# Kernel optimization log

Hardware: AMD Instinct MI355X
Metric: run time of the kernel (lower is better)

Reference implementation:

```python
import jax, jax.numpy as jnp
import numpy as np

H_DIM = 2048
D_FF = 4 * H_DIM
NUM_EXPERTS = 8
NUM_SHARED = 2
BATCH, SEQ = 2, 2048


def setup_inputs() -> dict:
    key = jax.random.key(0)
    ks = jax.random.split(key, 10)
    s = 0.02
    return {
        "x": jax.random.normal(ks[0], (BATCH, SEQ, H_DIM), dtype=jnp.float32),
        "ws_w1": jax.random.normal(ks[1], (NUM_SHARED, H_DIM, D_FF), dtype=jnp.float32) * s,
        "ws_b1": jnp.zeros((NUM_SHARED, D_FF), dtype=jnp.float32),
        "ws_w2": jax.random.normal(ks[2], (NUM_SHARED, D_FF, H_DIM), dtype=jnp.float32) * s,
        "ws_b2": jnp.zeros((NUM_SHARED, H_DIM), dtype=jnp.float32),
        "we_w1": jax.random.normal(ks[3], (NUM_EXPERTS, H_DIM, D_FF), dtype=jnp.float32) * s,
        "we_b1": jnp.zeros((NUM_EXPERTS, D_FF), dtype=jnp.float32),
        "we_w2": jax.random.normal(ks[4], (NUM_EXPERTS, D_FF, H_DIM), dtype=jnp.float32) * s,
        "we_b2": jnp.zeros((NUM_EXPERTS, H_DIM), dtype=jnp.float32),
        "wg": jax.random.normal(ks[5], (H_DIM, NUM_EXPERTS), dtype=jnp.float32) * s,
        "top_k": 2,
    }


def reference(x, ws_w1, ws_b1, ws_w2, ws_b2, we_w1, we_b1, we_w2, we_b2, wg, top_k):
    B, S, D = x.shape
    xt = x.reshape(-1, D)  # [T, D], T = B*S
    T = xt.shape[0]

    # ---- shared experts: sum over NUM_SHARED dense MLPs ----
    hs = jax.nn.relu(jnp.einsum('td,ndf->ntf', xt, ws_w1) + ws_b1[:, None, :])
    shared = jnp.einsum('ntf,nfd->td', hs, ws_w2) + ws_b2.sum(axis=0)  # [T, D]

    # ---- sparse top-k routed MoE ----
    logits = xt @ wg                       # [T, E] router logits
    probs = jax.nn.softmax(logits, axis=-1)
    topv, topi = jax.lax.top_k(probs, top_k)
    gates = jnp.zeros_like(probs).at[jnp.arange(T)[:, None], topi].set(topv)  # [T, E]

    moe = jnp.zeros_like(xt)
    for e in range(we_w1.shape[0]):  # small fixed expert count
        he = jax.nn.relu(xt @ we_w1[e] + we_b1[e])
        ye = he @ we_w2[e] + we_b2[e]
        moe = moe + gates[:, e:e + 1] * ye

    out = (shared + moe).reshape(B, S, D)
    return out, logits
```

## Files before the change

kernel.cpp:

```cpp
#include <hip/hip_runtime.h>

#define TOKENS 4096
#define HD 2048
#define FF 8192
#define NE 8
#define NS 2

typedef __attribute__((ext_vector_type(8))) short bf16x8;
typedef __attribute__((ext_vector_type(4))) float f32x4;

__device__ __forceinline__ unsigned rnd_bf(unsigned u) {
  return u + 0x7fffu + ((u >> 16) & 1u);
}
__device__ __forceinline__ unsigned short f2bf(float f) {
  unsigned u = __builtin_bit_cast(unsigned, f);
  return (unsigned short)(rnd_bf(u) >> 16);
}

#define GLDS16(gp, lp)                                                         \
  __builtin_amdgcn_global_load_lds(                                            \
      (const __attribute__((address_space(1))) unsigned*)(const void*)(gp),    \
      (__attribute__((address_space(3))) unsigned*)(lp), 16, 0, 0)

__global__ void cast_x_kernel(const float* __restrict__ x, unsigned short* __restrict__ xb) {
  const size_t i = ((size_t)blockIdx.x * 256 + threadIdx.x) * 4;
  float4 v = *(const float4*)(x + i);
  ushort4 o;
  o.x = f2bf(v.x); o.y = f2bf(v.y); o.z = f2bf(v.z); o.w = f2bf(v.w);
  *(ushort4*)(xb + i) = o;
}

__global__ void router_kernel(const float* __restrict__ x, const float* __restrict__ wg,
                              float* __restrict__ logits_out, int* __restrict__ topi,
                              float* __restrict__ topv, int* __restrict__ counts) {
  const int wave = threadIdx.x >> 6, lane = threadIdx.x & 63;
  const int t = blockIdx.x * 4 + wave;
  const float* xr = x + (size_t)t * HD;
  float acc[8];
#pragma unroll
  for (int e = 0; e < 8; ++e) acc[e] = 0.f;
  for (int d = lane; d < HD; d += 64) {
    const float xv = xr[d];
    const float4 w0 = *(const float4*)(wg + (size_t)d * 8);
    const float4 w1 = *(const float4*)(wg + (size_t)d * 8 + 4);
    acc[0] += xv * w0.x; acc[1] += xv * w0.y; acc[2] += xv * w0.z; acc[3] += xv * w0.w;
    acc[4] += xv * w1.x; acc[5] += xv * w1.y; acc[6] += xv * w1.z; acc[7] += xv * w1.w;
  }
#pragma unroll
  for (int e = 0; e < 8; ++e) {
#pragma unroll
    for (int off = 32; off > 0; off >>= 1) acc[e] += __shfl_xor(acc[e], off);
  }
  if (lane == 0) {
    *(float4*)(logits_out + (size_t)t * 8)     = make_float4(acc[0], acc[1], acc[2], acc[3]);
    *(float4*)(logits_out + (size_t)t * 8 + 4) = make_float4(acc[4], acc[5], acc[6], acc[7]);
    float mx = acc[0];
#pragma unroll
    for (int e = 1; e < 8; ++e) mx = fmaxf(mx, acc[e]);
    float p[8], s = 0.f;
#pragma unroll
    for (int e = 0; e < 8; ++e) { p[e] = expf(acc[e] - mx); s += p[e]; }
    const float inv = 1.f / s;
    int i1 = 0;
#pragma unroll
    for (int e = 1; e < 8; ++e) if (acc[e] > acc[i1]) i1 = e;
    int i2 = (i1 == 0) ? 1 : 0;
#pragma unroll
    for (int e = 0; e < 8; ++e) if (e != i1 && acc[e] > acc[i2]) i2 = e;
    topi[2 * t]     = i1; topv[2 * t]     = p[i1] * inv;
    topi[2 * t + 1] = i2; topv[2 * t + 1] = p[i2] * inv;
    atomicAdd(&counts[i1], 1);
    atomicAdd(&counts[i2], 1);
  }
}

__global__ void offs_kernel(const int* __restrict__ counts, int* __restrict__ offs,
                            int* __restrict__ cursors) {
  if (threadIdx.x == 0) {
    int r = 0;
    for (int e = 0; e < NE; ++e) { offs[e] = r; cursors[e] = r; r += counts[e]; }
  }
}

__global__ void gather_kernel(const unsigned short* __restrict__ xb,
                              const int* __restrict__ topi, const float* __restrict__ topv,
                              int* __restrict__ cursors, unsigned short* __restrict__ xg,
                              int* __restrict__ row_token, float* __restrict__ row_gate) {
  const int wave = threadIdx.x >> 6, lane = threadIdx.x & 63;
  const int t = blockIdx.x * 4 + wave;
  const uint4* src = (const uint4*)(xb + (size_t)t * HD);
#pragma unroll
  for (int j = 0; j < 2; ++j) {
    const int e = topi[2 * t + j];
    int pos = 0;
    if (lane == 0) {
      pos = atomicAdd(&cursors[e], 1);
      row_token[pos] = t;
      row_gate[pos] = topv[2 * t + j];
    }
    pos = __shfl(pos, 0);
    uint4* dst = (uint4*)(xg + (size_t)pos * HD);
#pragma unroll
    for (int c = lane; c < 256; c += 64) dst[c] = src[c];
  }
}

template <int K, int N>
__global__ __launch_bounds__(256) void pack_wt(const float* __restrict__ we,
                                               const float* __restrict__ ws,
                                               unsigned short* __restrict__ dstw) {
  const int e = blockIdx.z;
  const float* src = (e < NE) ? (we + (size_t)e * K * N) : (ws + (size_t)(e - NE) * K * N);
  unsigned short* dst = dstw + (size_t)e * K * N;
  const int nt = blockIdx.x * 64;
  const int kt = blockIdx.y * 64;
  __shared__ unsigned short t[64][73];
  const int tid = threadIdx.x;
  const int rr = tid >> 4, cc = (tid & 15) * 4;
#pragma unroll
  for (int i = 0; i < 4; ++i) {
    const int k = rr + i * 16;
    float4 v = *(const float4*)(src + (size_t)(kt + k) * N + nt + cc);
    t[k][cc + 0] = f2bf(v.x);
    t[k][cc + 1] = f2bf(v.y);
    t[k][cc + 2] = f2bf(v.z);
    t[k][cc + 3] = f2bf(v.w);
  }
  __syncthreads();
  const int nr = tid >> 2, kc = (tid & 3) * 16;
  unsigned u[8];
#pragma unroll
  for (int j = 0; j < 8; ++j)
    u[j] = (unsigned)t[kc + 2 * j][nr] | ((unsigned)t[kc + 2 * j + 1][nr] << 16);
  unsigned short* dp = dst + (size_t)(nt + nr) * K + kt + kc;
  uint4 v0; v0.x = u[0]; v0.y = u[1]; v0.z = u[2]; v0.w = u[3];
  uint4 v1; v1.x = u[4]; v1.y = u[5]; v1.z = u[6]; v1.w = u[7];
  *(uint4*)dp = v0;
  *(uint4*)(dp + 8) = v1;
}

template <int MS>
__device__ __forceinline__ void rd_a(bf16x8 (&d)[8], const unsigned short* base,
                                     int wr, int fr, int fq, int swz) {
#pragma unroll
  for (int mi = 0; mi < 4; ++mi)
#pragma unroll
    for (int ks = 0; ks < 2; ++ks)
      d[mi * 2 + ks] = *(const bf16x8*)(base + (wr * 128 + MS * 64 + mi * 16 + fr) * 64 +
                                        (((ks * 4 + fq) ^ swz) << 3));
}
template <int NSUB>
__device__ __forceinline__ void rd_b(bf16x8 (&d)[4], const unsigned short* base,
                                     int wc, int fr, int fq, int swz) {
#pragma unroll
  for (int ni = 0; ni < 2; ++ni)
#pragma unroll
    for (int ks = 0; ks < 2; ++ks)
      d[ni * 2 + ks] = *(const bf16x8*)(base + (wc * 64 + NSUB * 32 + ni * 16 + fr) * 64 +
                                        (((ks * 4 + fq) ^ swz) << 3));
}
template <int MS, int NSUB>
__device__ __forceinline__ void mm16(f32x4 (&acc)[8][4], const bf16x8 (&a)[8],
                                     const bf16x8 (&b)[4]) {
  __builtin_amdgcn_s_setprio(1);
#pragma unroll
  for (int mi = 0; mi < 4; ++mi)
#pragma unroll
    for (int ni = 0; ni < 2; ++ni)
#pragma unroll
      for (int ks = 0; ks < 2; ++ks)
        acc[MS * 4 + mi][NSUB * 2 + ni] = __builtin_amdgcn_mfma_f32_16x16x32_bf16(
            a[mi * 2 + ks], b[ni * 2 + ks], acc[MS * 4 + mi][NSUB * 2 + ni], 0, 0, 0);
  __builtin_amdgcn_s_setprio(0);
}

#define PH_BAR_PRE()                                                           \
  __builtin_amdgcn_sched_barrier(0);                                           \
  __builtin_amdgcn_s_barrier();                                                \
  asm volatile("s_waitcnt lgkmcnt(0)" ::: "memory");                           \
  __builtin_amdgcn_sched_barrier(0)
#define PH_BAR_POST()                                                          \
  __builtin_amdgcn_sched_barrier(0);                                           \
  __builtin_amdgcn_s_barrier()

template <int MODE>
__global__ __launch_bounds__(512, 2) void gemm8p(
    const unsigned short* __restrict__ Ash,
    const unsigned short* __restrict__ Art,
    const unsigned short* __restrict__ wt,
    const float* __restrict__ bE, const float* __restrict__ bS,
    unsigned short* __restrict__ hout, float* __restrict__ out,
    const int* __restrict__ counts, const int* __restrict__ offs,
    const int* __restrict__ row_token, const float* __restrict__ row_gate) {
  constexpr int K = (MODE == 0) ? HD : FF;
  constexpr int N = (MODE == 0) ? FF : HD;
  constexpr int NBX = N / 256;
  constexpr int NWG = NBX * 16;
  extern __shared__ unsigned short smem[];

  const int e = blockIdx.z;
  int M;
  const unsigned short* A;
  const float* bias;
  int hbase = 0;
  const int* tok = nullptr;
  const float* gt = nullptr;

  if (e < NE) {
    M = counts[e];
    const int off = offs[e];
    A = Art + (size_t)off * K;
    if (MODE == 1) { tok = row_token + off; gt = row_gate + off; }
    bias = bE + (size_t)e * N;
    hbase = off;
  } else {
    M = TOKENS;
    const int se = e - NE;
    hbase = 2 * TOKENS + se * TOKENS;
    if (MODE == 0) A = Ash;
    else           A = Ash + (size_t)hbase * K;
    bias = bS + (size_t)se * N;
  }
  const unsigned short* Bt = wt + (size_t)e * HD * FF;

  int flat = blockIdx.x + NBX * blockIdx.y;
  flat = (flat & 7) * (NWG >> 3) + (flat >> 3);
  const int m0 = (flat & 15) * 256;
  const int n0 = (flat >> 4) * 256;
  if (m0 >= M) return;

  const int tid = threadIdx.x;
  const int wid = tid >> 6, ln = tid & 63;
  const int wr = wid >> 2, wc = wid & 3;
  const int fr = ln & 15, fq = ln >> 4;
  const int swz = fr & 7;

  const int lr8 = ln >> 3;
  const int lc8 = ln & 7;
  const int scol = (lc8 ^ lr8) << 3;
  const int wrA = wr * 128 + wc * 16;
  const int wcB = wc * 64 + wr * 16;

#define SA(s, kt, b)                                                           \
  { const int r0_ = wrA + (s) * 64 + lr8;                                      \
    const unsigned short* s_ = A + (size_t)(m0 + r0_) * K + (kt) * 64 + scol;  \
    unsigned short* d_ = smem + (b) * 32768 + r0_ * 64 + lc8 * 8;              \
    GLDS16(s_, d_); GLDS16(s_ + (size_t)8 * K, d_ + 8 * 64); }
#define SB(s, kt, b)                                                           \
  { const int r0_ = wcB + (s) * 32 + lr8;                                      \
    const unsigned short* s_ = Bt + (size_t)(n0 + r0_) * K + (kt) * 64 + scol; \
    unsigned short* d_ = smem + (b) * 32768 + 16384 + r0_ * 64 + lc8 * 8;      \
    GLDS16(s_, d_); GLDS16(s_ + (size_t)8 * K, d_ + 8 * 64); }

  f32x4 acc[8][4];
#pragma unroll
  for (int i = 0; i < 8; ++i)
#pragma unroll
    for (int j = 0; j < 4; ++j) acc[i][j] = (f32x4){0.f, 0.f, 0.f, 0.f};

  SA(0, 0, 0); SA(1, 0, 0); SB(0, 0, 0); SB(1, 0, 0);
  SA(0, 1, 1); SA(1, 1, 1); SB(0, 1, 1); SB(1, 1, 1);
  asm volatile("s_waitcnt vmcnt(8)" ::: "memory");
  __builtin_amdgcn_s_barrier();

  bf16x8 a0[8], a1[8], b0[4], b1[4];
  const int nkt = K / 64;
  for (int t = 0; t < nkt; ++t) {
    const int cur = t & 1;
    const int tp2 = (t + 2 < nkt) ? t + 2 : t;
    const unsigned short* As_c = smem + cur * 32768;
    const unsigned short* Bs_c = As_c + 16384;
    rd_a<0>(a0, As_c, wr, fr, fq, swz);
    rd_b<0>(b0, Bs_c, wc, fr, fq, swz);
    asm volatile("s_waitcnt lgkmcnt(8)" ::: "memory");
    PH_BAR_PRE();
    mm16<0, 0>(acc, a0, b0);
    PH_BAR_POST();
    rd_b<1>(b1, Bs_c, wc, fr, fq, swz);
    SA(0, tp2, cur); SB(0, tp2, cur);
    PH_BAR_PRE();
    mm16<0, 1>(acc, a0, b1);
    PH_BAR_POST();
    rd_a<1>(a1, As_c, wr, fr, fq, swz);
    SB(1, tp2, cur);
    PH_BAR_PRE();
    mm16<1, 1>(acc, a1, b1);
    PH_BAR_POST();
    SA(1, tp2, cur);
    __builtin_amdgcn_sched_barrier(0);
    __builtin_amdgcn_s_barrier();
    __builtin_amdgcn_sched_barrier(0);
    mm16<1, 0>(acc, a1, b0);
    __builtin_amdgcn_sched_barrier(0);
    asm volatile("s_waitcnt vmcnt(8)" ::: "memory");
    __builtin_amdgcn_s_barrier();
  }
#undef SA
#undef SB

  if (MODE == 0) {
#pragma unroll
    for (int nn = 0; nn < 4; ++nn) {
      const int col = n0 + wc * 64 + (nn >> 1) * 32 + (nn & 1) * 16 + fr;
      const float bb = bias[col];
#pragma unroll
      for (int mm = 0; mm < 8; ++mm) {
#pragma unroll
        for (int j = 0; j < 4; ++j) {
          const int r = m0 + wr * 128 + (mm >> 2) * 64 + (mm & 3) * 16 + fq * 4 + j;
          if (r < M) {
            float v = acc[mm][nn][j] + bb;
            v = v > 0.f ? v : 0.f;
            hout[(size_t)(hbase + r) * FF + col] = f2bf(v);
          }
        }
      }
    }
  } else {
#pragma unroll
    for (int mm = 0; mm < 8; ++mm) {
#pragma unroll
      for (int j = 0; j < 4; ++j) {
        const int r = m0 + wr * 128 + (mm >> 2) * 64 + (mm & 3) * 16 + fq * 4 + j;
        if (r < M) {
          const int t = tok ? tok[r] : r;
          const float g = gt ? gt[r] : 1.f;
          float* orow = out + (size_t)t * HD + n0;
#pragma unroll
          for (int nn = 0; nn < 4; ++nn) {
            const int col = wc * 64 + (nn >> 1) * 32 + (nn & 1) * 16 + fr;
            atomicAdd(orow + col, g * (acc[mm][nn][j] + bias[n0 + col]));
          }
        }
      }
    }
  }
}

extern "C" void kernel_launch(void* const* d_in, const int* in_sizes, int n_in,
                              void* d_out, int out_size, void* d_ws, size_t ws_size,
                              hipStream_t stream) {
  const float* x     = (const float*)d_in[0];
  const float* ws_w1 = (const float*)d_in[1];
  const float* ws_b1 = (const float*)d_in[2];
  const float* ws_w2 = (const float*)d_in[3];
  const float* ws_b2 = (const float*)d_in[4];
  const float* we_w1 = (const float*)d_in[5];
  const float* we_b1 = (const float*)d_in[6];
  const float* we_w2 = (const float*)d_in[7];
  const float* we_b2 = (const float*)d_in[8];
  const float* wg    = (const float*)d_in[9];

  float* out = (float*)d_out;
  float* logits = out + (size_t)TOKENS * HD;

  char* ws = (char*)d_ws;
  unsigned short* wt   = (unsigned short*)ws;
  unsigned short* xb   = (unsigned short*)(ws + 335544320);
  unsigned short* xg   = (unsigned short*)(ws + 352321536);
  unsigned short* hbuf = (unsigned short*)(ws + 386400256);
  char* ctrl = ws + 654835712;
  int*   row_token = (int*)(ctrl);
  float* row_gate  = (float*)(ctrl + 32768);
  int*   topi      = (int*)(ctrl + 65536);
  float* topv      = (float*)(ctrl + 98304);
  int*   counts    = (int*)(ctrl + 131072);
  int*   offs      = (int*)(ctrl + 131104);
  int*   cursors   = (int*)(ctrl + 131136);

  hipFuncSetAttribute(reinterpret_cast<const void*>(gemm8p<0>),
                      hipFuncAttributeMaxDynamicSharedMemorySize, 131072);
  hipFuncSetAttribute(reinterpret_cast<const void*>(gemm8p<1>),
                      hipFuncAttributeMaxDynamicSharedMemorySize, 131072);

  hipMemsetAsync(out, 0, (size_t)TOKENS * HD * sizeof(float), stream);
  hipMemsetAsync(counts, 0, NE * sizeof(int), stream);

  cast_x_kernel<<<8192, 256, 0, stream>>>(x, xb);
  router_kernel<<<1024, 256, 0, stream>>>(x, wg, logits, topi, topv, counts);
  offs_kernel<<<1, 64, 0, stream>>>(counts, offs, cursors);
  gather_kernel<<<1024, 256, 0, stream>>>(xb, topi, topv, cursors, xg, row_token, row_gate);

  pack_wt<HD, FF><<<dim3(FF / 64, HD / 64, 10), 256, 0, stream>>>(we_w1, ws_w1, wt);
  gemm8p<0><<<dim3(32, 16, 10), 512, 131072, stream>>>(
      xb, xg, wt, we_b1, ws_b1, hbuf, nullptr, counts, offs, nullptr, nullptr);
  pack_wt<FF, HD><<<dim3(HD / 64, FF / 64, 10), 256, 0, stream>>>(we_w2, ws_w2, wt);
  gemm8p<1><<<dim3(8, 16, 10), 512, 131072, stream>>>(
      hbuf, hbuf, wt, we_b2, ws_b2, nullptr, out, counts, offs, row_token, row_gate);

  (void)in_sizes; (void)n_in; (void)out_size; (void)ws_size;
}
```

Before: 2.077 ms.

## Split GEMM kernels; merge shared-expert down-projections into one K-concatenated pass

The first GEMM becomes its own kernel with a two-phase inner schedule: all B fragments are read up front and each phase issues 32 MFMAs, halving the barrier phases per k-tile. The second GEMM now folds the two shared experts into a single z-slice that walks a concatenated K of 16384, switching A and B pointers at the midpoint and summing both biases. This removes a full set of fp32 atomicAdd passes over the output and reduces barrier overhead. In exchange, the shared z-slice has twice the serial K length, which may create a long tail, and the first GEMM needs more registers live at once.

New measurement: 2.076 ms. No clear change (-0.0%).

```diff
diff --git a/kernel.cpp b/kernel.cpp
--- a/kernel.cpp
+++ b/kernel.cpp
@@ -173,6 +173,22 @@
             a[mi * 2 + ks], b[ni * 2 + ks], acc[MS * 4 + mi][NSUB * 2 + ni], 0, 0, 0);
   __builtin_amdgcn_s_setprio(0);
 }
+template <int MS>
+__device__ __forceinline__ void mm32(f32x4 (&acc)[8][4], const bf16x8 (&a)[8],
+                                     const bf16x8 (&b0)[4], const bf16x8 (&b1)[4]) {
+  __builtin_amdgcn_s_setprio(1);
+#pragma unroll
+  for (int mi = 0; mi < 4; ++mi)
+#pragma unroll
+    for (int nn = 0; nn < 4; ++nn)
+#pragma unroll
+      for (int ks = 0; ks < 2; ++ks) {
+        const bf16x8& bb = (nn < 2) ? b0[(nn & 1) * 2 + ks] : b1[(nn & 1) * 2 + ks];
+        acc[MS * 4 + mi][nn] = __builtin_amdgcn_mfma_f32_16x16x32_bf16(
+            a[mi * 2 + ks], bb, acc[MS * 4 + mi][nn], 0, 0, 0);
+      }
+  __builtin_amdgcn_s_setprio(0);
+}
 
 #define PH_BAR_PRE()                                                           \
   __builtin_amdgcn_sched_barrier(0);                                           \
@@ -183,18 +199,15 @@
   __builtin_amdgcn_sched_barrier(0);                                           \
   __builtin_amdgcn_s_barrier()
 
-template <int MODE>
-__global__ __launch_bounds__(512, 2) void gemm8p(
+__global__ __launch_bounds__(512, 2) void gemm2p(
     const unsigned short* __restrict__ Ash,
     const unsigned short* __restrict__ Art,
     const unsigned short* __restrict__ wt,
     const float* __restrict__ bE, const float* __restrict__ bS,
-    unsigned short* __restrict__ hout, float* __restrict__ out,
-    const int* __restrict__ counts, const int* __restrict__ offs,
-    const int* __restrict__ row_token, const float* __restrict__ row_gate) {
-  constexpr int K = (MODE == 0) ? HD : FF;
-  constexpr int N = (MODE == 0) ? FF : HD;
-  constexpr int NBX = N / 256;
+    unsigned short* __restrict__ hout,
+    const int* __restrict__ counts, const int* __restrict__ offs) {
+  constexpr int K = HD;
+  constexpr int NBX = FF / 256;
   constexpr int NWG = NBX * 16;
   extern __shared__ unsigned short smem[];
 
@@ -202,24 +215,17 @@
   int M;
   const unsigned short* A;
   const float* bias;
-  int hbase = 0;
-  const int* tok = nullptr;
-  const float* gt = nullptr;
-
+  int hbase;
   if (e < NE) {
     M = counts[e];
-    const int off = offs[e];
-    A = Art + (size_t)off * K;
-    if (MODE == 1) { tok = row_token + off; gt = row_gate + off; }
-    bias = bE + (size_t)e * N;
-    hbase = off;
+    A = Art + (size_t)offs[e] * K;
+    bias = bE + (size_t)e * FF;
+    hbase = offs[e];
   } else {
     M = TOKENS;
-    const int se = e - NE;
-    hbase = 2 * TOKENS + se * TOKENS;
-    if (MODE == 0) A = Ash;
-    else           A = Ash + (size_t)hbase * K;
-    bias = bS + (size_t)se * N;
+    A = Ash;
+    bias = bS + (size_t)(e - NE) * FF;
+    hbase = 2 * TOKENS + (e - NE) * TOKENS;
   }
   const unsigned short* Bt = wt + (size_t)e * HD * FF;
 
@@ -265,6 +271,134 @@
 
   bf16x8 a0[8], a1[8], b0[4], b1[4];
   const int nkt = K / 64;
+  for (int t = 0; t < nkt; ++t) {
+    const int cur = t & 1;
+    const int tp2 = (t + 2 < nkt) ? t + 2 : t;
+    const unsigned short* As_c = smem + cur * 32768;
+    const unsigned short* Bs_c = As_c + 16384;
+    rd_a<0>(a0, As_c, wr, fr, fq, swz);
+    rd_b<0>(b0, Bs_c, wc, fr, fq, swz);
+    rd_b<1>(b1, Bs_c, wc, fr, fq, swz);
+    asm volatile("s_waitcnt lgkmcnt(8)" ::: "memory");
+    PH_BAR_PRE();
+    mm32<0>(acc, a0, b0, b1);
+    PH_BAR_POST();
+    rd_a<1>(a1, As_c, wr, fr, fq, swz);
+    SB(0, tp2, cur); SB(1, tp2, cur);
+    PH_BAR_PRE();
+    mm32<1>(acc, a1, b1, b0);
+    __builtin_amdgcn_sched_barrier(0);
+    SA(0, tp2, cur); SA(1, tp2, cur);
+    __builtin_amdgcn_sched_barrier(0);
+    asm volatile("s_waitcnt vmcnt(8)" ::: "memory");
+    __builtin_amdgcn_s_barrier();
+  }
+#undef SA
+#undef SB
+
+#pragma unroll
+  for (int nn = 0; nn < 4; ++nn) {
+#pragma unroll
+    for (int mm = 0; mm < 8; ++mm) {
+      const int nsub_lo = (mm < 4) ? (nn >> 1) : 1 - (nn >> 1);
+      const int col = n0 + wc * 64 + nsub_lo * 32 + (nn & 1) * 16 + fr;
+      const float bb = bias[col];
+#pragma unroll
+      for (int j = 0; j < 4; ++j) {
+        const int r = m0 + wr * 128 + (mm >> 2) * 64 + (mm & 3) * 16 + fq * 4 + j;
+        if (r < M) {
+          float v = acc[mm][nn][j] + bb;
+          v = v > 0.f ? v : 0.f;
+          hout[(size_t)(hbase + r) * FF + col] = f2bf(v);
+        }
+      }
+    }
+  }
+}
+
+__global__ __launch_bounds__(512, 2) void gemm8p(
+    const unsigned short* __restrict__ hbuf,
+    const unsigned short* __restrict__ wt,
+    const float* __restrict__ bE, const float* __restrict__ bS,
+    float* __restrict__ out,
+    const int* __restrict__ counts, const int* __restrict__ offs,
+    const int* __restrict__ row_token, const float* __restrict__ row_gate) {
+  constexpr int K = FF;
+  constexpr int NBX = HD / 256;
+  constexpr int NWG = NBX * 16;
+  extern __shared__ unsigned short smem[];
+
+  const int e = blockIdx.z;
+  const bool merged = (e == NE);
+  int M;
+  const unsigned short *A, *A2;
+  const unsigned short *B, *B2;
+  const float *bias, *bias2;
+  const int* tok = nullptr;
+  const float* gt = nullptr;
+
+  if (!merged) {
+    M = counts[e];
+    const int off = offs[e];
+    A = hbuf + (size_t)off * K;  A2 = A;
+    tok = row_token + off; gt = row_gate + off;
+    B = wt + (size_t)e * HD * FF;  B2 = B;
+    bias = bE + (size_t)e * HD;  bias2 = bias;
+  } else {
+    M = TOKENS;
+    A  = hbuf + (size_t)(2 * TOKENS) * K;
+    A2 = hbuf + (size_t)(3 * TOKENS) * K;
+    B  = wt + (size_t)NE * HD * FF;
+    B2 = wt + (size_t)(NE + 1) * HD * FF;
+    bias = bS;  bias2 = bS + HD;
+  }
+
+  int flat = blockIdx.x + NBX * blockIdx.y;
+  flat = (flat & 7) * (NWG >> 3) + (flat >> 3);
+  const int m0 = (flat & 15) * 256;
+  const int n0 = (flat >> 4) * 256;
+  if (m0 >= M) return;
+
+  const int tid = threadIdx.x;
+  const int wid = tid >> 6, ln = tid & 63;
+  const int wr = wid >> 2, wc = wid & 3;
+  const int fr = ln & 15, fq = ln >> 4;
+  const int swz = fr & 7;
+
+  const int lr8 = ln >> 3;
+  const int lc8 = ln & 7;
+  const int scol = (lc8 ^ lr8) << 3;
+  const int wrA = wr * 128 + wc * 16;
+  const int wcB = wc * 64 + wr * 16;
+
+#define SA(s, kt, b)                                                           \
+  { int kl_ = (kt); const unsigned short* ab_ = A;                             \
+    if (merged && kl_ >= 128) { ab_ = A2; kl_ -= 128; }                        \
+    const int r0_ = wrA + (s) * 64 + lr8;                                      \
+    const unsigned short* s_ = ab_ + (size_t)(m0 + r0_) * K + kl_ * 64 + scol; \
+    unsigned short* d_ = smem + (b) * 32768 + r0_ * 64 + lc8 * 8;              \
+    GLDS16(s_, d_); GLDS16(s_ + (size_t)8 * K, d_ + 8 * 64); }
+#define SB(s, kt, b)                                                           \
+  { int kl_ = (kt); const unsigned short* bb_ = B;                             \
+    if (merged && kl_ >= 128) { bb_ = B2; kl_ -= 128; }                        \
+    const int r0_ = wcB + (s) * 32 + lr8;                                      \
+    const unsigned short* s_ = bb_ + (size_t)(n0 + r0_) * K + kl_ * 64 + scol; \
+    unsigned short* d_ = smem + (b) * 32768 + 16384 + r0_ * 64 + lc8 * 8;      \
+    GLDS16(s_, d_); GLDS16(s_ + (size_t)8 * K, d_ + 8 * 64); }
+
+  f32x4 acc[8][4];
+#pragma unroll
+  for (int i = 0; i < 8; ++i)
+#pragma unroll
+    for (int j = 0; j < 4; ++j) acc[i][j] = (f32x4){0.f, 0.f, 0.f, 0.f};
+
+  SA(0, 0, 0); SA(1, 0, 0); SB(0, 0, 0); SB(1, 0, 0);
+  SA(0, 1, 1); SA(1, 1, 1); SB(0, 1, 1); SB(1, 1, 1);
+  asm volatile("s_waitcnt vmcnt(8)" ::: "memory");
+  __builtin_amdgcn_s_barrier();
+
+  bf16x8 a0[8], a1[8], b0[4], b1[4];
+  const int nkt = merged ? 256 : 128;
   for (int t = 0; t < nkt; ++t) {
     const int cur = t & 1;
     const int tp2 = (t + 2 < nkt) ? t + 2 : t;
@@ -298,39 +432,21 @@
 #undef SA
 #undef SB
 
-  if (MODE == 0) {
-#pragma unroll
-    for (int nn = 0; nn < 4; ++nn) {
-      const int col = n0 + wc * 64 + (nn >> 1) * 32 + (nn & 1) * 16 + fr;
-      const float bb = bias[col];
-#pragma unroll
-      for (int mm = 0; mm < 8; ++mm) {
-#pragma unroll
-        for (int j = 0; j < 4; ++j) {
-          const int r = m0 + wr * 128 + (mm >> 2) * 64 + (mm & 3) * 16 + fq * 4 + j;
-          if (r < M) {
-            float v = acc[mm][nn][j] + bb;
-            v = v > 0.f ? v : 0.f;
-            hout[(size_t)(hbase + r) * FF + col] = f2bf(v);
-          }
-        }
-      }
-    }
-  } else {
-#pragma unroll
-    for (int mm = 0; mm < 8; ++mm) {
-#pragma unroll
-      for (int j = 0; j < 4; ++j) {
-        const int r = m0 + wr * 128 + (mm >> 2) * 64 + (mm & 3) * 16 + fq * 4 + j;
-        if (r < M) {
-          const int t = tok ? tok[r] : r;
-          const float g = gt ? gt[r] : 1.f;
-          float* orow = out + (size_t)t * HD + n0;
-#pragma unroll
-          for (int nn = 0; nn < 4; ++nn) {
-            const int col = wc * 64 + (nn >> 1) * 32 + (nn & 1) * 16 + fr;
-            atomicAdd(orow + col, g * (acc[mm][nn][j] + bias[n0 + col]));
-          }
+#pragma unroll
+  for (int mm = 0; mm < 8; ++mm) {
+#pragma unroll
+    for (int j = 0; j < 4; ++j) {
+      const int r = m0 + wr * 128 + (mm >> 2) * 64 + (mm & 3) * 16 + fq * 4 + j;
+      if (r < M) {
+        const int t = tok ? tok[r] : r;
+        const float g = gt ? gt[r] : 1.f;
+        float* orow = out + (size_t)t * HD + n0;
+#pragma unroll
+        for (int nn = 0; nn < 4; ++nn) {
+          const int col = wc * 64 + (nn >> 1) * 32 + (nn & 1) * 16 + fr;
+          float bb = bias[n0 + col];
+          if (merged) bb += bias2[n0 + col];
+          atomicAdd(orow + col, g * (acc[mm][nn][j] + bb));
         }
       }
     }
@@ -368,9 +484,9 @@
   int*   offs      = (int*)(ctrl + 131104);
   int*   cursors   = (int*)(ctrl + 131136);
 
-  hipFuncSetAttribute(reinterpret_cast<const void*>(gemm8p<0>),
+  hipFuncSetAttribute(reinterpret_cast<const void*>(gemm2p),
                       hipFuncAttributeMaxDynamicSharedMemorySize, 131072);
-  hipFuncSetAttribute(reinterpret_cast<const void*>(gemm8p<1>),
+  hipFuncSetAttribute(reinterpret_cast<const void*>(gemm8p),
                       hipFuncAttributeMaxDynamicSharedMemorySize, 131072);
 
   hipMemsetAsync(out, 0, (size_t)TOKENS * HD * sizeof(float), stream);
@@ -382,11 +498,11 @@
   gather_kernel<<<1024, 256, 0, stream>>>(xb, topi, topv, cursors, xg, row_token, row_gate);
 
   pack_wt<HD, FF><<<dim3(FF / 64, HD / 64, 10), 256, 0, stream>>>(we_w1, ws_w1, wt);
-  gemm8p<0><<<dim3(32, 16, 10), 512, 131072, stream>>>(
-      xb, xg, wt, we_b1, ws_b1, hbuf, nullptr, counts, offs, nullptr, nullptr);
+  gemm2p<<<dim3(32, 16, 10), 512, 131072, stream>>>(
+      xb, xg, wt, we_b1, ws_b1, hbuf, counts, offs);
   pack_wt<FF, HD><<<dim3(HD / 64, FF / 64, 10), 256, 0, stream>>>(we_w2, ws_w2, wt);
-  gemm8p<1><<<dim3(8, 16, 10), 512, 131072, stream>>>(
-      hbuf, hbuf, wt, we_b2, ws_b2, nullptr, out, counts, offs, row_token, row_gate);
+  gemm8p<<<dim3(8, 16, 9), 512, 131072, stream>>>(
+      hbuf, wt, we_b2, ws_b2, out, counts, offs, row_token, row_gate);
 
   (void)in_sizes; (void)n_in; (void)out_size; (void)ws_size;
 }
```
